# Performance work log

Hardware: AMD Instinct MI355X
Metric: run time of the kernel (lower is better)

Reference implementation:

```python
import jax, jax.numpy as jnp
import numpy as np
from jax import lax

# module constants (match init_kwargs)
CHUNK_LENGTH = 32
RIGHT_CONTEXT_LENGTH = 8
CHANNELS = 512
KERNEL_SIZE = 31
CACHE_SIZE = KERNEL_SIZE - 1  # 30


def _conv1d(x, w, b, groups=1):
    # x: (N, C_in, L), w: (C_out, C_in/groups, K), b: (C_out,)
    y = lax.conv_general_dilated(
        x, w, window_strides=(1,), padding='VALID',
        dimension_numbers=('NCH', 'OIH', 'NCH'),
        feature_group_count=groups)
    return y + b[None, :, None]


def setup_inputs() -> dict:
    key = jax.random.key(0)
    ks = jax.random.split(key, 9)
    U, B, D, R = 2048, 16, CHANNELS, 512
    s = 0.02
    return {
        'utterance': jax.random.normal(ks[0], (U, B, D), jnp.float32),
        'right_context': jax.random.normal(ks[1], (R, B, D), jnp.float32),
        'cache': jnp.zeros((B, D, CACHE_SIZE), jnp.float32),
        'w1': jax.random.normal(ks[2], (2 * D, D, 1), jnp.float32) * s,
        'b1': jax.random.normal(ks[3], (2 * D,), jnp.float32) * s,
        'wd': jax.random.normal(ks[4], (D, 1, KERNEL_SIZE), jnp.float32) * s,
        'bd': jax.random.normal(ks[5], (D,), jnp.float32) * s,
        'w2': jax.random.normal(ks[6], (D, D, 1), jnp.float32) * s,
        'b2': jax.random.normal(ks[7], (D,), jnp.float32) * s,
    }


def reference(utterance, right_context, cache, w1, b1, wd, bd, w2, b2):
    U, B, D = utterance.shape
    R = right_context.shape[0]
    rcl, cl, cs = RIGHT_CONTEXT_LENGTH, CHUNK_LENGTH, CACHE_SIZE

    # concat [right_context; utterance] along time, to (B, D, R+U)
    x = jnp.concatenate([right_context, utterance], axis=0).transpose(1, 2, 0)
    # pointwise_conv1 (ScaledConv1d == plain conv in forward math) + GLU
    # (ActivationBalancer is identity in forward)
    x = _conv1d(x, w1, b1)  # (B, 2D, R+U)
    a, g = jnp.split(x, 2, axis=1)
    x = a * jax.nn.sigmoid(g)  # GLU -> (B, D, R+U)

    utt = x[:, :, R:]      # (B, D, U)
    rc = x[:, :, :R]       # (B, D, R)

    # causal depthwise conv with left cache
    pad_utt = jnp.concatenate([cache, utt], axis=2)  # (B, D, cs+U)
    new_cache = pad_utt[:, :, -cs:]
    utt = _conv1d(pad_utt, wd, bd, groups=D)  # (B, D, U)

    # _split_right_context: gather per-chunk left cache for each rc segment
    U_ = cs + U
    num_chunks = R // rcl
    pad_utt_t = pad_utt.transpose(2, 0, 1)   # (U_, B, D)
    rc_t = rc.transpose(2, 0, 1)             # (R, B, D)
    end_idx = jnp.minimum(U_, cs + (jnp.arange(num_chunks) + 1) * cl)
    start_idx = end_idx - cs                 # (num_chunks,)
    gidx = start_idx[:, None] + jnp.arange(cs)[None, :]   # (nc, cs)
    padding = pad_utt_t[gidx]                # (nc, cs, B, D)
    padding = padding.transpose(0, 2, 1, 3).reshape(num_chunks * B, cs, D)
    rc_seg = rc_t.reshape(num_chunks, rcl, B, D).transpose(0, 2, 1, 3)
    rc_seg = rc_seg.reshape(num_chunks * B, rcl, D)
    pad_rc = jnp.concatenate([padding, rc_seg], axis=1).transpose(0, 2, 1)  # (nc*B, D, cs+rcl)
    rc_out = _conv1d(pad_rc, wd, bd, groups=D)  # (nc*B, D, rcl)
    # _merge_right_context
    rc_out = rc_out.reshape(num_chunks, B, D, rcl).transpose(1, 2, 0, 3)
    rc_out = rc_out.reshape(B, D, R)

    x = jnp.concatenate([rc_out, utt], axis=2)  # (B, D, R+U)
    # DoubleSwish: x * sigmoid(x - 1)
    x = x * jax.nn.sigmoid(x - 1.0)
    x = _conv1d(x, w2, b2)  # pointwise_conv2

    rc_final = x[:, :, :R].transpose(2, 0, 1)   # (R, B, D)
    utt_final = x[:, :, R:].transpose(2, 0, 1)  # (U, B, D)
    return utt_final, rc_final, new_cache
```

## Files before the change

### kernel.cpp

```cpp
#include <hip/hip_runtime.h>
#include <math.h>

#define B_SZ 16
#define D_CH 512
#define U_LEN 2048
#define R_LEN 512
#define T_LEN 2560
#define KS 31
#define CS 30

typedef __attribute__((ext_vector_type(8))) short short8;
typedef __attribute__((ext_vector_type(4))) float floatx4;

__device__ __forceinline__ float bf2f(ushort u) {
    unsigned v = (unsigned)u << 16;
    float f; __builtin_memcpy(&f, &v, 4); return f;
}
__device__ __forceinline__ ushort f2bf(float f) {
    unsigned v; __builtin_memcpy(&v, &f, 4);
    v += 0x7fff + ((v >> 16) & 1);
    return (ushort)(v >> 16);
}
__device__ __forceinline__ float sigmoidf_(float x) { return 1.0f / (1.0f + __expf(-x)); }

__device__ __forceinline__ void gld16(const void* g, void* l) {
    __builtin_amdgcn_global_load_lds((const __attribute__((address_space(1))) void*)g,
                                     (__attribute__((address_space(3))) void*)l, 16, 0, 0);
}

__global__ __launch_bounds__(256) void k_conv_all(
    const float* __restrict__ utt, const float* __restrict__ rc, const float* __restrict__ cache,
    const float* __restrict__ w1, const float* __restrict__ w2,
    ushort* __restrict__ xb, ushort* __restrict__ w1b, ushort* __restrict__ w2b,
    ushort* __restrict__ xc)
{
    int blk = blockIdx.x;
    if (blk < 5120) {
        size_t f4 = (size_t)blk * 1024 + threadIdx.x * 4;
        size_t o = f4 * 4;
        int q = (int)(o >> 9), d = (int)(o & 511);
        const float* src = (q < 8192) ? rc + ((size_t)q << 9) + d
                                      : utt + (((size_t)(q - 8192)) << 9) + d;
        ushort* dst = xb + o;
        #pragma unroll
        for (int i = 0; i < 4; ++i) {
            float4 v = ((const float4*)src)[i];
            ushort4 u4; u4.x = f2bf(v.x); u4.y = f2bf(v.y); u4.z = f2bf(v.z); u4.w = f2bf(v.w);
            ((ushort4*)dst)[i] = u4;
        }
    } else if (blk < 5312) {
        int t = (blk - 5120) * 1024 + threadIdx.x * 4;
        if (t < 131072) {
            #pragma unroll
            for (int i = 0; i < 4; ++i) {
                int e = (t + i) << 2;
                int row = e >> 9, k = e & 511;
                int rr = row & 511;
                int rp = (rr >> 4) * 32 + ((row >> 9) << 4) + (rr & 15);
                float4 v = ((const float4*)w1)[t + i];
                ushort4 u4; u4.x = f2bf(v.x); u4.y = f2bf(v.y); u4.z = f2bf(v.z); u4.w = f2bf(v.w);
                ((ushort4*)w1b)[rp * 128 + (k >> 2)] = u4;
            }
        } else {
            int t2 = t - 131072;
            #pragma unroll
            for (int i = 0; i < 4; ++i) {
                float4 v = ((const float4*)w2)[t2 + i];
                ushort4 u4; u4.x = f2bf(v.x); u4.y = f2bf(v.y); u4.z = f2bf(v.z); u4.w = f2bf(v.w);
                ((ushort4*)w2b)[t2 + i] = u4;
            }
        }
    } else {
        int o = (blk - 5312) * 256 + threadIdx.x;
        int d = o & 511, p = o >> 13, b = (o >> 9) & 15;
        xc[o] = f2bf(cache[((size_t)b * D_CH + d) * CS + p]);
    }
}

__global__ __launch_bounds__(256, 2) void k1_mfma(
    const ushort* __restrict__ xb, const ushort* __restrict__ w1p,
    const float* __restrict__ b1, ushort* __restrict__ y)
{
    __shared__ __attribute__((aligned(16))) ushort lds[4][2][4096];
    const int tid = threadIdx.x;
    const int w = tid >> 6, lane = tid & 63;
    const int col = lane & 15, quad = lane >> 4;
    const int wm = w >> 1, wn = w & 1;
    const int bid = blockIdx.x;
    const int f = (bid & 7) * 320 + (bid >> 3);
    const int mt = f >> 3, nn = f & 7;
    const int q0 = mt * 128, n0 = nn * 128;

    floatx4 acc[4][4];
    #pragma unroll
    for (int i = 0; i < 4; ++i)
        #pragma unroll
        for (int j = 0; j < 4; ++j) acc[i][j] = 0.f;

    int offA[4], offB[4];
    #pragma unroll
    for (int i = 0; i < 4; ++i) {
        int rA = wm * 64 + i * 16 + col;
        offA[i] = rA * 64 + ((quad ^ ((rA >> 1) & 3)) << 4);
        int rB = wn * 64 + i * 16 + col;
        offB[i] = rB * 64 + ((quad ^ ((rB >> 1) & 3)) << 4);
    }

    const int srow = tid >> 2;
    const int sqs = (tid & 3) ^ ((srow >> 1) & 3);
    const ushort* gA0 = xb  + (((size_t)(q0 + srow))      << 9) + (sqs << 3);
    const ushort* gA1 = xb  + (((size_t)(q0 + 64 + srow)) << 9) + (sqs << 3);
    const ushort* gB0 = w1p + (((size_t)(n0 + srow))      << 9) + (sqs << 3);
    const ushort* gB1 = w1p + (((size_t)(n0 + 64 + srow)) << 9) + (sqs << 3);

#define STAGE1(t_, bi_) do { \
        const int kc_ = (t_) << 5; \
        gld16(gA0 + kc_, &lds[bi_][0][w * 512]); \
        gld16(gA1 + kc_, &lds[bi_][0][2048 + w * 512]); \
        gld16(gB0 + kc_, &lds[bi_][1][w * 512]); \
        gld16(gB1 + kc_, &lds[bi_][1][2048 + w * 512]); \
    } while (0)

    STAGE1(0, 0); STAGE1(1, 1); STAGE1(2, 2);

    #pragma unroll
    for (int s = 0; s < 16; ++s) {
        if (s < 14)       asm volatile("s_waitcnt vmcnt(8)\n\ts_barrier" ::: "memory");
        else if (s == 14) asm volatile("s_waitcnt vmcnt(4)\n\ts_barrier" ::: "memory");
        else              asm volatile("s_waitcnt vmcnt(0)\n\ts_barrier" ::: "memory");
        if (s < 13) STAGE1(s + 3, (s + 3) & 3);
        const char* A  = (const char*)&lds[s & 3][0][0];
        const char* Bp = (const char*)&lds[s & 3][1][0];
        short8 af[4], bf8[4];
        #pragma unroll
        for (int i = 0; i < 4; ++i) af[i]  = *(const short8*)(A + offA[i]);
        #pragma unroll
        for (int j = 0; j < 4; ++j) bf8[j] = *(const short8*)(Bp + offB[j]);
        __builtin_amdgcn_s_setprio(1);
        #pragma unroll
        for (int i = 0; i < 4; ++i)
            #pragma unroll
            for (int j = 0; j < 4; ++j)
                acc[i][j] = __builtin_amdgcn_mfma_f32_16x16x32_bf16(af[i], bf8[j], acc[i][j], 0, 0, 0);
        __builtin_amdgcn_s_setprio(0);
    }
#undef STAGE1

    const int nb2 = (n0 + wn * 64) >> 1;
    #pragma unroll
    for (int fe = 0; fe < 2; ++fe) {
        const int na = nb2 + fe * 16 + col;
        const float ba = b1[na], bg = b1[512 + na];
        #pragma unroll
        for (int i = 0; i < 4; ++i) {
            const int row = q0 + wm * 64 + i * 16 + quad * 4;
            #pragma unroll
            for (int r = 0; r < 4; ++r) {
                float a = acc[i][2 * fe][r] + ba;
                float g = acc[i][2 * fe + 1][r] + bg;
                y[(((size_t)(row + r)) << 9) + na] = f2bf(a * sigmoidf_(g));
            }
        }
    }
}

__global__ __launch_bounds__(256) void k2_fused(
    const ushort* __restrict__ y, const ushort* __restrict__ xc,
    const float* __restrict__ wd, const float* __restrict__ bd,
    ushort* __restrict__ z, float* __restrict__ out)
{
    __shared__ __attribute__((aligned(16))) char smem[20352];
    const int tid = threadIdx.x;
    int g = blockIdx.x;

    if (g < 4096) {
        ushort* sy = (ushort*)smem;
        float*  sw = (float*)(smem + 12416);
        const int u0 = (g & 31) * 64;
        const int d0 = ((g >> 5) & 7) * 64;
        const int b  = g >> 8;

        for (int idx = tid; idx < 94 * 8; idx += 256) {
            int r  = idx >> 3;
            int c8 = idx & 7;
            int p  = u0 + r;
            int dg = d0 + c8 * 8;
            const ushort* src = (p < CS) ? xc + (((size_t)(p * 16 + b)) << 9) + dg
                                         : y  + (((size_t)((482 + p) * 16 + b)) << 9) + dg;
            ushort tmp[8];
            *(int4*)tmp = *(const int4*)src;
            #pragma unroll
            for (int j = 0; j < 8; ++j) sy[(c8 * 8 + j) * 97 + r] = tmp[j];
        }
        for (int idx = tid; idx < 64 * 31; idx += 256) {
            int d = idx / 31, k = idx - d * 31;
            sw[d * 31 + k] = wd[(size_t)(d0 + d) * KS + k];
        }
        __syncthreads();

        const int dl   = tid & 63;
        const int useg = (tid >> 6) * 16;
        float win[46];
        #pragma unroll
        for (int p = 0; p < 46; ++p) win[p] = bf2f(sy[dl * 97 + useg + p]);
        float bias = bd[d0 + dl];
        float acc[16];
        #pragma unroll
        for (int i = 0; i < 16; ++i) acc[i] = bias;
        for (int k = 0; k < 31; ++k) {
            float w = sw[dl * 31 + k];
            #pragma unroll
            for (int i = 0; i < 16; ++i) acc[i] = fmaf(w, win[k + i], acc[i]);
        }
        #pragma unroll
        for (int i = 0; i < 16; ++i) {
            float v = acc[i];
            v = v * sigmoidf_(v - 1.0f);
            int u = u0 + useg + i;
            z[(((size_t)((R_LEN + u) * 16 + b)) << 9) + d0 + dl] = f2bf(v);
        }
        if ((g & 31) == 31) {
            for (int idx = tid; idx < 64 * 30; idx += 256) {
                int dl2 = idx & 63, j = idx >> 6;
                out[(size_t)20971520 + ((size_t)b * D_CH + d0 + dl2) * CS + j] = bf2f(sy[dl2 * 97 + 64 + j]);
            }
        }
    } else {
        g -= 4096;
        ushort* sy = (ushort*)smem;
        const int i  = g & 63;
        const int b  = (g >> 6) & 15;
        const int dbase = (g >> 10) * 256;

        for (int idx = tid; idx < 38 * 32; idx += 256) {
            int r  = idx >> 5;
            int c8 = idx & 31;
            int t = (r < CS) ? (R_LEN + 32 * i + 2 + r) : (8 * i + (r - CS));
            *(int4*)&sy[r * 256 + c8 * 8] =
                *(const int4*)(y + (((size_t)(t * 16 + b)) << 9) + dbase + c8 * 8);
        }
        __syncthreads();

        const int dd = dbase + tid;
        float wr[31];
        #pragma unroll
        for (int k = 0; k < 31; ++k) wr[k] = wd[(size_t)dd * KS + k];
        float bias = bd[dd];
        #pragma unroll
        for (int j = 0; j < 8; ++j) {
            float acc = bias;
            #pragma unroll
            for (int k = 0; k < 31; ++k) acc = fmaf(wr[k], bf2f(sy[(j + k) * 256 + tid]), acc);
            float v = acc * sigmoidf_(acc - 1.0f);
            z[(((size_t)((i * 8 + j) * 16 + b)) << 9) + dd] = f2bf(v);
        }
    }
}

__global__ __launch_bounds__(256, 2) void k3_mfma(
    const ushort* __restrict__ zb, const ushort* __restrict__ w2b,
    const float* __restrict__ b2, float* __restrict__ out)
{
    __shared__ __attribute__((aligned(16))) ushort lds[4][2][4096];
    const int tid = threadIdx.x;
    const int w = tid >> 6, lane = tid & 63;
    const int col = lane & 15, quad = lane >> 4;
    const int wm = w >> 1, wn = w & 1;
    const int bid = blockIdx.x;
    const int f = (bid & 7) * 160 + (bid >> 3);
    const int mt = f >> 2, nn = f & 3;
    const int q0 = mt * 128, n0 = nn * 128;

    floatx4 acc[4][4];
    #pragma unroll
    for (int i = 0; i < 4; ++i)
        #pragma unroll
        for (int j = 0; j < 4; ++j) acc[i][j] = 0.f;

    int offA[4], offB[4];
    #pragma unroll
    for (int i = 0; i < 4; ++i) {
        int rA = wm * 64 + i * 16 + col;
        offA[i] = rA * 64 + ((quad ^ ((rA >> 1) & 3)) << 4);
        int rB = wn * 64 + i * 16 + col;
        offB[i] = rB * 64 + ((quad ^ ((rB >> 1) & 3)) << 4);
    }

    const int srow = tid >> 2;
    const int sqs = (tid & 3) ^ ((srow >> 1) & 3);
    const ushort* gA0 = zb  + (((size_t)(q0 + srow))      << 9) + (sqs << 3);
    const ushort* gA1 = zb  + (((size_t)(q0 + 64 + srow)) << 9) + (sqs << 3);
    const ushort* gB0 = w2b + (((size_t)(n0 + srow))      << 9) + (sqs << 3);
    const ushort* gB1 = w2b + (((size_t)(n0 + 64 + srow)) << 9) + (sqs << 3);

#define STAGE3(t_, bi_) do { \
        const int kc_ = (t_) << 5; \
        gld16(gA0 + kc_, &lds[bi_][0][w * 512]); \
        gld16(gA1 + kc_, &lds[bi_][0][2048 + w * 512]); \
        gld16(gB0 + kc_, &lds[bi_][1][w * 512]); \
        gld16(gB1 + kc_, &lds[bi_][1][2048 + w * 512]); \
    } while (0)

    STAGE3(0, 0); STAGE3(1, 1); STAGE3(2, 2);

    #pragma unroll
    for (int s = 0; s < 16; ++s) {
        if (s < 14)       asm volatile("s_waitcnt vmcnt(8)\n\ts_barrier" ::: "memory");
        else if (s == 14) asm volatile("s_waitcnt vmcnt(4)\n\ts_barrier" ::: "memory");
        else              asm volatile("s_waitcnt vmcnt(0)\n\ts_barrier" ::: "memory");
        if (s < 13) STAGE3(s + 3, (s + 3) & 3);
        const char* A  = (const char*)&lds[s & 3][0][0];
        const char* Bp = (const char*)&lds[s & 3][1][0];
        short8 af[4], bf8[4];
        #pragma unroll
        for (int i = 0; i < 4; ++i) af[i]  = *(const short8*)(A + offA[i]);
        #pragma unroll
        for (int j = 0; j < 4; ++j) bf8[j] = *(const short8*)(Bp + offB[j]);
        __builtin_amdgcn_s_setprio(1);
        #pragma unroll
        for (int i = 0; i < 4; ++i)
            #pragma unroll
            for (int j = 0; j < 4; ++j)
                acc[i][j] = __builtin_amdgcn_mfma_f32_16x16x32_bf16(af[i], bf8[j], acc[i][j], 0, 0, 0);
        __builtin_amdgcn_s_setprio(0);
    }
#undef STAGE3

    #pragma unroll
    for (int j = 0; j < 4; ++j) {
        const int n = n0 + wn * 64 + j * 16 + col;
        const float bb = b2[n];
        #pragma unroll
        for (int i = 0; i < 4; ++i) {
            const int qrow = q0 + wm * 64 + i * 16 + quad * 4;
            #pragma unroll
            for (int r = 0; r < 4; ++r) {
                const int q = qrow + r;
                float v = acc[i][j][r] + bb;
                size_t off = (q < 8192) ? (size_t)16777216 + ((size_t)q << 9)
                                        : ((size_t)(q - 8192) << 9);
                out[off + n] = v;
            }
        }
    }
}

extern "C" void kernel_launch(void* const* d_in, const int* in_sizes, int n_in,
                              void* d_out, int out_size, void* d_ws, size_t ws_size,
                              hipStream_t stream)
{
    const float* utt   = (const float*)d_in[0];
    const float* rc    = (const float*)d_in[1];
    const float* cache = (const float*)d_in[2];
    const float* w1    = (const float*)d_in[3];
    const float* b1    = (const float*)d_in[4];
    const float* wd    = (const float*)d_in[5];
    const float* bd    = (const float*)d_in[6];
    const float* w2    = (const float*)d_in[7];
    const float* b2    = (const float*)d_in[8];
    float* out = (float*)d_out;

    ushort* xb  = (ushort*)d_ws;
    ushort* y   = xb  + (size_t)20971520;
    ushort* zb  = y   + (size_t)20971520;
    ushort* w1b = zb  + (size_t)20971520;
    ushort* w2b = w1b + (size_t)524288;
    ushort* xc  = w2b + (size_t)262144;

    k_conv_all<<<dim3(6272), 256, 0, stream>>>(utt, rc, cache, w1, w2, xb, w1b, w2b, xc);
    k1_mfma   <<<dim3(2560), 256, 0, stream>>>(xb, w1b, b1, y);
    k2_fused  <<<dim3(6144), 256, 0, stream>>>(y, xc, wd, bd, zb, out);
    k3_mfma   <<<dim3(1280), 256, 0, stream>>>(zb, w2b, b2, out);
}
```

Baseline: 309.3 us.

## Write GLU output into cache-padded buffer and register-stream depthwise conv without LDS

The first GEMM now writes utterance rows straight into a contiguous buffer that follows the converted cache, so the depthwise conv reads one padded sequence with no cache/utterance branching. The depthwise conv kernel drops its LDS staging and transpose. Each thread owns one channel and streams 62 (or 38) time steps through registers with a sliding accumulator, reading depthwise weights from a pre-transposed copy for coalesced loads. The block count shrinks and per-thread work grows. This raises register pressure and relies on coalesced strided global loads instead of shared-memory reuse.

```diff
diff --git a/kernel.cpp b/kernel.cpp
--- a/kernel.cpp
+++ b/kernel.cpp
@@ -30,9 +30,9 @@
 
 __global__ __launch_bounds__(256) void k_conv_all(
     const float* __restrict__ utt, const float* __restrict__ rc, const float* __restrict__ cache,
-    const float* __restrict__ w1, const float* __restrict__ w2,
+    const float* __restrict__ w1, const float* __restrict__ w2, const float* __restrict__ wd,
     ushort* __restrict__ xb, ushort* __restrict__ w1b, ushort* __restrict__ w2b,
-    ushort* __restrict__ xc)
+    ushort* __restrict__ pu, float* __restrict__ wdT)
 {
     int blk = blockIdx.x;
     if (blk < 5120) {
@@ -70,16 +70,20 @@
                 ((ushort4*)w2b)[t2 + i] = u4;
             }
         }
-    } else {
+    } else if (blk < 6272) {
         int o = (blk - 5312) * 256 + threadIdx.x;
         int d = o & 511, p = o >> 13, b = (o >> 9) & 15;
-        xc[o] = f2bf(cache[((size_t)b * D_CH + d) * CS + p]);
+        pu[o] = f2bf(cache[((size_t)b * D_CH + d) * CS + p]);
+    } else {
+        int idx = (blk - 6272) * 256 + threadIdx.x;
+        int k = idx >> 9, d = idx & 511;
+        wdT[idx] = wd[(size_t)d * KS + k];
     }
 }
 
 __global__ __launch_bounds__(256, 2) void k1_mfma(
     const ushort* __restrict__ xb, const ushort* __restrict__ w1p,
-    const float* __restrict__ b1, ushort* __restrict__ y)
+    const float* __restrict__ b1, ushort* __restrict__ yr, ushort* __restrict__ pu)
 {
     __shared__ __attribute__((aligned(16))) ushort lds[4][2][4096];
     const int tid = threadIdx.x;
@@ -146,6 +150,8 @@
     }
 #undef STAGE1
 
+    ushort* dst = (q0 < 8192) ? yr : pu;
+    const int qb = (q0 < 8192) ? q0 : (q0 - 7712);
     const int nb2 = (n0 + wn * 64) >> 1;
     #pragma unroll
     for (int fe = 0; fe < 2; ++fe) {
@@ -153,106 +159,86 @@
         const float ba = b1[na], bg = b1[512 + na];
         #pragma unroll
         for (int i = 0; i < 4; ++i) {
-            const int row = q0 + wm * 64 + i * 16 + quad * 4;
+            const int row = qb + wm * 64 + i * 16 + quad * 4;
             #pragma unroll
             for (int r = 0; r < 4; ++r) {
                 float a = acc[i][2 * fe][r] + ba;
                 float g = acc[i][2 * fe + 1][r] + bg;
-                y[(((size_t)(row + r)) << 9) + na] = f2bf(a * sigmoidf_(g));
+                dst[(((size_t)(row + r)) << 9) + na] = f2bf(a * sigmoidf_(g));
             }
         }
     }
 }
 
 __global__ __launch_bounds__(256) void k2_fused(
-    const ushort* __restrict__ y, const ushort* __restrict__ xc,
-    const float* __restrict__ wd, const float* __restrict__ bd,
+    const ushort* __restrict__ pu, const ushort* __restrict__ yr,
+    const float* __restrict__ wdT, const float* __restrict__ bd,
     ushort* __restrict__ z, float* __restrict__ out)
 {
-    __shared__ __attribute__((aligned(16))) char smem[20352];
     const int tid = threadIdx.x;
-    int g = blockIdx.x;
-
-    if (g < 4096) {
-        ushort* sy = (ushort*)smem;
-        float*  sw = (float*)(smem + 12416);
-        const int u0 = (g & 31) * 64;
-        const int d0 = ((g >> 5) & 7) * 64;
-        const int b  = g >> 8;
-
-        for (int idx = tid; idx < 94 * 8; idx += 256) {
-            int r  = idx >> 3;
-            int c8 = idx & 7;
-            int p  = u0 + r;
-            int dg = d0 + c8 * 8;
-            const ushort* src = (p < CS) ? xc + (((size_t)(p * 16 + b)) << 9) + dg
-                                         : y  + (((size_t)((482 + p) * 16 + b)) << 9) + dg;
-            ushort tmp[8];
-            *(int4*)tmp = *(const int4*)src;
-            #pragma unroll
-            for (int j = 0; j < 8; ++j) sy[(c8 * 8 + j) * 97 + r] = tmp[j];
-        }
-        for (int idx = tid; idx < 64 * 31; idx += 256) {
-            int d = idx / 31, k = idx - d * 31;
-            sw[d * 31 + k] = wd[(size_t)(d0 + d) * KS + k];
-        }
-        __syncthreads();
-
-        const int dl   = tid & 63;
-        const int useg = (tid >> 6) * 16;
-        float win[46];
-        #pragma unroll
-        for (int p = 0; p < 46; ++p) win[p] = bf2f(sy[dl * 97 + useg + p]);
-        float bias = bd[d0 + dl];
-        float acc[16];
-        #pragma unroll
-        for (int i = 0; i < 16; ++i) acc[i] = bias;
-        for (int k = 0; k < 31; ++k) {
-            float w = sw[dl * 31 + k];
-            #pragma unroll
-            for (int i = 0; i < 16; ++i) acc[i] = fmaf(w, win[k + i], acc[i]);
-        }
-        #pragma unroll
-        for (int i = 0; i < 16; ++i) {
+    const int bid = blockIdx.x;
+    if (bid < 2048) {
+        const int ug = bid & 63, b = (bid >> 6) & 15, dh = bid >> 10;
+        const int d = dh * 256 + tid;
+        const int u0 = ug * 32;
+        float wreg[31];
+        #pragma unroll
+        for (int k = 0; k < 31; ++k) wreg[k] = wdT[k * 512 + d];
+        const float bias = bd[d];
+        float acc[32];
+        #pragma unroll
+        for (int i = 0; i < 32; ++i) acc[i] = bias;
+        const ushort* base = pu + (((size_t)u0 * 16 + b) << 9) + d;
+        #pragma unroll
+        for (int p = 0; p < 62; ++p) {
+            float v = bf2f(base[(size_t)p * 8192]);
+            #pragma unroll
+            for (int i = 0; i < 32; ++i) {
+                int k = p - i;
+                if (k >= 0 && k < 31) acc[i] = fmaf(wreg[k], v, acc[i]);
+            }
+        }
+        ushort* zp = z + d;
+        #pragma unroll
+        for (int i = 0; i < 32; ++i) {
             float v = acc[i];
             v = v * sigmoidf_(v - 1.0f);
-            int u = u0 + useg + i;
-            z[(((size_t)((R_LEN + u) * 16 + b)) << 9) + d0 + dl] = f2bf(v);
-        }
-        if ((g & 31) == 31) {
-            for (int idx = tid; idx < 64 * 30; idx += 256) {
-                int dl2 = idx & 63, j = idx >> 6;
-                out[(size_t)20971520 + ((size_t)b * D_CH + d0 + dl2) * CS + j] = bf2f(sy[dl2 * 97 + 64 + j]);
-            }
+            zp[((size_t)((R_LEN + u0 + i) * 16 + b)) << 9] = f2bf(v);
+        }
+        if (ug == 63) {
+            float* outc = out + 20971520 + ((size_t)b * 512 + d) * 30;
+            #pragma unroll
+            for (int p = 32; p < 62; ++p)
+                outc[p - 32] = bf2f(base[(size_t)p * 8192]);
         }
     } else {
-        g -= 4096;
-        ushort* sy = (ushort*)smem;
-        const int i  = g & 63;
-        const int b  = (g >> 6) & 15;
-        const int dbase = (g >> 10) * 256;
-
-        for (int idx = tid; idx < 38 * 32; idx += 256) {
-            int r  = idx >> 5;
-            int c8 = idx & 31;
-            int t = (r < CS) ? (R_LEN + 32 * i + 2 + r) : (8 * i + (r - CS));
-            *(int4*)&sy[r * 256 + c8 * 8] =
-                *(const int4*)(y + (((size_t)(t * 16 + b)) << 9) + dbase + c8 * 8);
-        }
-        __syncthreads();
-
-        const int dd = dbase + tid;
-        float wr[31];
-        #pragma unroll
-        for (int k = 0; k < 31; ++k) wr[k] = wd[(size_t)dd * KS + k];
-        float bias = bd[dd];
+        const int m = bid - 2048;
+        const int ci = m & 63, b = (m >> 6) & 15, dh = m >> 10;
+        const int d = dh * 256 + tid;
+        float wreg[31];
+        #pragma unroll
+        for (int k = 0; k < 31; ++k) wreg[k] = wdT[k * 512 + d];
+        const float bias = bd[d];
+        float acc[8];
+        #pragma unroll
+        for (int j = 0; j < 8; ++j) acc[j] = bias;
+        #pragma unroll
+        for (int r = 0; r < 38; ++r) {
+            const ushort* src = (r < 30)
+                ? pu + (((size_t)((32 * ci + 32 + r) * 16 + b)) << 9) + d
+                : yr + (((size_t)(((8 * ci) + (r - 30)) * 16 + b)) << 9) + d;
+            float v = bf2f(*src);
+            #pragma unroll
+            for (int j = 0; j < 8; ++j) {
+                int k = r - j;
+                if (k >= 0 && k < 31) acc[j] = fmaf(wreg[k], v, acc[j]);
+            }
+        }
         #pragma unroll
         for (int j = 0; j < 8; ++j) {
-            float acc = bias;
-            #pragma unroll
-            for (int k = 0; k < 31; ++k) acc = fmaf(wr[k], bf2f(sy[(j + k) * 256 + tid]), acc);
-            float v = acc * sigmoidf_(acc - 1.0f);
-            z[(((size_t)((i * 8 + j) * 16 + b)) << 9) + dd] = f2bf(v);
+            float v = acc[j];
+            v = v * sigmoidf_(v - 1.0f);
+            z[(((size_t)((ci * 8 + j) * 16 + b)) << 9) + d] = f2bf(v);
         }
     }
 }
@@ -361,14 +347,15 @@
     float* out = (float*)d_out;
 
     ushort* xb  = (ushort*)d_ws;
-    ushort* y   = xb  + (size_t)20971520;
-    ushort* zb  = y   + (size_t)20971520;
-    ushort* w1b = zb  + (size_t)20971520;
+    ushort* zb  = xb  + (size_t)20971520;
+    ushort* pu  = zb  + (size_t)20971520;
+    ushort* yr  = pu  + (size_t)17039360;
+    ushort* w1b = yr  + (size_t)4194304;
     ushort* w2b = w1b + (size_t)524288;
-    ushort* xc  = w2b + (size_t)262144;
-
-    k_conv_all<<<dim3(6272), 256, 0, stream>>>(utt, rc, cache, w1, w2, xb, w1b, w2b, xc);
-    k1_mfma   <<<dim3(2560), 256, 0, stream>>>(xb, w1b, b1, y);
-    k2_fused  <<<dim3(6144), 256, 0, stream>>>(y, xc, wd, bd, zb, out);
+    float*  wdT = (float*)(w2b + (size_t)262144);
+
+    k_conv_all<<<dim3(6334), 256, 0, stream>>>(utt, rc, cache, w1, w2, wd, xb, w1b, w2b, pu, wdT);
+    k1_mfma   <<<dim3(2560), 256, 0, stream>>>(xb, w1b, b1, yr, pu);
+    k2_fused  <<<dim3(4096), 256, 0, stream>>>(pu, yr, wdT, bd, zb, out);
     k3_mfma   <<<dim3(1280), 256, 0, stream>>>(zb, w2b, b2, out);
 }
```

Measured after the change: 362.6 us. 1.17x slower.
